# Kernel tuning notes

Hardware: AMD Instinct MI355X
Metric: run time of the kernel (lower is better)

Reference implementation:

```python
import jax, jax.numpy as jnp
import numpy as np

T, B, N = 12, 2, 1024
M = B * N            # nodes per timestep (batch-flattened)
D_IN, D_H, D_T, D_O = 64, 128, 16, 32


def _linear_params(k, fin, fout):
    kw, kb = jax.random.split(k)
    s = 1.0 / np.sqrt(fin)
    w = jax.random.uniform(kw, (fin, fout), jnp.float32, -s, s)
    b = jax.random.uniform(kb, (fout,), jnp.float32, -s, s)
    return w, b


def setup_inputs() -> dict:
    key = jax.random.key(0)
    ks = jax.random.split(key, 12)
    x = jax.random.normal(ks[0], (T, M, D_IN), jnp.float32)
    A = (jax.random.uniform(ks[1], (T, M, M)) < 0.01).astype(jnp.float32)
    A = A * (1.0 - jnp.eye(M, dtype=jnp.float32))  # no self-loops in raw adjacency
    ego_mask = jax.random.randint(ks[2], (B, T, N), 0, 2).astype(bool)
    gcn1_w, gcn1_b = _linear_params(ks[3], D_IN, D_H)
    gcn2_w, gcn2_b = _linear_params(ks[4], D_H, D_H)
    time_w, time_b = _linear_params(ks[5], 1, D_T)
    q_w, q_b = _linear_params(ks[6], D_H + D_T, D_H)
    k_w, k_b = _linear_params(ks[7], D_H + D_T, D_H)
    v_w, v_b = _linear_params(ks[8], D_H + D_T, D_H)
    o_w, o_b = _linear_params(ks[9], D_H, D_H)
    fc_w, fc_b = _linear_params(ks[10], D_H, D_O)
    return dict(x=x, A=A, ego_mask=ego_mask,
                gcn1_w=gcn1_w, gcn1_b=gcn1_b, gcn2_w=gcn2_w, gcn2_b=gcn2_b,
                time_w=time_w, time_b=time_b,
                q_w=q_w, q_b=q_b, k_w=k_w, k_b=k_b, v_w=v_w, v_b=v_b,
                o_w=o_w, o_b=o_b, fc_w=fc_w, fc_b=fc_b)


def _forward(x, A, ego_mask, gcn1_w, gcn1_b, gcn2_w, gcn2_b, time_w, time_b,
             q_w, q_b, k_w, k_b, v_w, v_b, o_w, o_b, fc_w, fc_b):
    # [B,T,N] -> [T, B*N], as in mask.permute(1,0,2).reshape(T,-1)
    mask = ego_mask.transpose(1, 0, 2).reshape(T, M)
    tvals = jnp.arange(T, dtype=jnp.float32)

    def step(_, inp):
        xt, At, mt, tv = inp  # [M,D_IN], [M,M], [M] bool, scalar
        m = mt.astype(xt.dtype)
        # restrict adjacency to masked subgraph; GCNConv adds self-loops
        A_hat = At * (m[:, None] * m[None, :]) + jnp.diag(m)
        deg = A_hat.sum(axis=0)  # in-degree per target (PyG gcn_norm on col)
        nrm = jnp.where(deg > 0, 1.0 / jnp.sqrt(jnp.maximum(deg, 1e-12)), 0.0)

        def gcn(h, w, b):
            # out[i] = nrm[i] * sum_j A_hat[j,i] * nrm[j] * (hW)[j] + b
            return (A_hat.T @ ((h @ w) * nrm[:, None])) * nrm[:, None] + b

        h = jax.nn.relu(gcn(xt, gcn1_w, gcn1_b))
        h = jax.nn.relu(gcn(h, gcn2_w, gcn2_b))
        # t_vec = sin(Linear(1,D_T)(t)) -- identical for all nodes
        t_vec = jnp.sin(tv * time_w[0] + time_b)  # [D_T]
        xtc = jnp.concatenate([h, jnp.broadcast_to(t_vec, (M, D_T))], axis=-1)
        Q = xtc @ q_w + q_b
        K = xtc @ k_w + k_b
        V = xtc @ v_w + v_b
        scores = (Q @ K.T) * (1.0 / np.sqrt(D_H))  # [M,M]
        scores = jnp.where(mt[None, :], scores, -1e9)  # keys restricted to mask
        agg = jax.nn.softmax(scores, axis=-1) @ V
        out = ((agg @ o_w + o_b) @ fc_w + fc_b) * m[:, None]  # scatter-back == mask
        return None, out

    _, outs = jax.lax.scan(step, None, (x, A, mask, tvals))  # [T,M,D_O]
    return outs.reshape(T, B, N, D_O).transpose(1, 2, 0, 3)  # [B,N,T,D_O]


def reference(x, A, ego_mask, gcn1_w, gcn1_b, gcn2_w, gcn2_b, time_w, time_b,
              q_w, q_b, k_w, k_b, v_w, v_b, o_w, o_b, fc_w, fc_b):
    return _forward(x, A, ego_mask, gcn1_w, gcn1_b, gcn2_w, gcn2_b, time_w,
                    time_b, q_w, q_b, k_w, k_b, v_w, v_b, o_w, o_b, fc_w, fc_b)
```

## Files before the change

kernel.cpp:

```cpp
#include <hip/hip_runtime.h>
#include <stdint.h>

#define TT   12
#define BB   2
#define NN   1024
#define MM   2048
#define TM   24576
#define DIN  64
#define DH   128
#define DOUT 32
#define CAP  64
#define OUTSZ 786432
#define KS   4
#define PWB  324

typedef __attribute__((ext_vector_type(8))) short short8;
typedef __attribute__((ext_vector_type(4))) short short4v;
typedef __attribute__((ext_vector_type(4))) float f32x4;

#define MFMA(a,b,c) __builtin_amdgcn_mfma_f32_16x16x32_bf16((a),(b),(c),0,0,0)

__device__ __forceinline__ float bf2f(unsigned short u){
  union { uint32_t i; float f; } x; x.i = ((uint32_t)u) << 16; return x.f;
}
__device__ __forceinline__ unsigned short f2bf(float f){
  union { float f; uint32_t i; } x; x.f = f;
  uint32_t u = x.i + 0x7FFFu + ((x.i >> 16) & 1u);
  return (unsigned short)(u >> 16);
}
__device__ __forceinline__ float LD(const void* p, size_t i, int mode){
  return mode ? ((const float*)p)[i] : bf2f(((const unsigned short*)p)[i]);
}
__device__ __forceinline__ short8 ldx8(const void* x, size_t off, int md){
  if(md){
    const float4* xf = (const float4*)((const float*)x + off);
    float4 a = xf[0], b = xf[1];
    short8 o;
    o[0]=(short)f2bf(a.x); o[1]=(short)f2bf(a.y); o[2]=(short)f2bf(a.z); o[3]=(short)f2bf(a.w);
    o[4]=(short)f2bf(b.x); o[5]=(short)f2bf(b.y); o[6]=(short)f2bf(b.z); o[7]=(short)f2bf(b.w);
    return o;
  }
  return *(const short8*)((const unsigned short*)x + off);
}

__global__ void k_fill(float* __restrict__ out, int n, float val){
  int i = blockIdx.x*blockDim.x + threadIdx.x;
  if(i < n) out[i] = val;
}

__global__ void k_detect2(const unsigned short* __restrict__ x,
                          const unsigned char* __restrict__ eg,
                          int* __restrict__ dtf, int* __restrict__ flag,
                          int* __restrict__ nact){
  if(blockIdx.x == 0){
    __shared__ int cnt_s;
    if(threadIdx.x==0) cnt_s = 0;
    if(threadIdx.x < TT) nact[threadIdx.x] = 0;
    __syncthreads();
    int c = 0;
    for(int i=threadIdx.x; i<6144; i+=blockDim.x){
      unsigned short h = x[i*2];
      unsigned e = (h >> 7) & 0xFF;
      if(h==0 || (e >= 0x60 && e <= 0x9F)) c++;
    }
    atomicAdd(&cnt_s, c);
    __syncthreads();
    if(threadIdx.x==0) *dtf = (cnt_s > 4000) ? 0 : 1;
  } else {
    __shared__ int pres_s, ge2_s;
    if(threadIdx.x==0){ pres_s=0; ge2_s=0; }
    __syncthreads();
    int pres=0, ge2=0;
    for(int i=threadIdx.x; i<24576; i+=blockDim.x){
      unsigned v = eg[i];
      if(v){ pres |= 1 << (i & 7); if(v >= 2u) ge2 = 1; }
    }
    if(pres) atomicOr(&pres_s, pres);
    if(ge2)  atomicOr(&ge2_s, 1);
    __syncthreads();
    if(threadIdx.x==0){
      int pr = pres_s, g2 = ge2_s, mode;
      if(!g2){
        if((pr & ~0x01) == 0)      mode = 4;
        else if((pr & ~0x11) == 0) mode = 0;
        else                       mode = 1;
      } else {
        if((pr & ~0xC0) == 0)      mode = 5;
        else if((pr & ~0xCC) == 0) mode = 3;
        else                       mode = 2;
      }
      *flag = mode;
    }
  }
}

__global__ void k_mask(const void* __restrict__ egom, const int* __restrict__ flag,
                       int* __restrict__ cnt, int* __restrict__ nact,
                       int* __restrict__ aidx, int* __restrict__ inv,
                       float* __restrict__ out){
  int idx = blockIdx.x*blockDim.x + threadIdx.x;
  out[idx] = 0.f;
  if(idx >= TM) return;
  int t = idx / MM, node = idx % MM;
  int b = node / NN, n = node % NN;
  int src = (b*TT + t)*NN + n;
  int mode = *flag;
  int v;
  if(mode==0)      v = ((const int*)egom)[src] != 0;
  else if(mode==1) v = ((const unsigned char*)egom)[src] != 0;
  else if(mode==2) v = ((const unsigned short*)egom)[src] != 0;
  else if(mode==3) v = ((const float*)egom)[src] != 0.f;
  else if(mode==4) v = ((const long long*)egom)[src] != 0;
  else             v = ((const double*)egom)[src] != 0.0;
  cnt[idx] = 0;
  unsigned long long bal = __ballot(v != 0);
  int lane = threadIdx.x & 63;
  int base = 0;
  if(lane == 0 && bal) base = atomicAdd(&nact[t], __popcll(bal));
  base = __shfl(base, 0, 64);
  int ic = -1;
  if(v){
    int pfx = __popcll(bal & ((1ULL << lane) - 1ULL));
    ic = base + pfx;
    aidx[(size_t)t*MM + ic] = node;
  }
  inv[idx] = ic;
}

__global__ __launch_bounds__(256) void k_prep_edges(
  const void* __restrict__ w1, const void* __restrict__ w2,
  const void* __restrict__ qw, const void* __restrict__ kw, const void* __restrict__ vw,
  const void* __restrict__ qb0, const void* __restrict__ kb0, const void* __restrict__ vb0,
  const void* __restrict__ ow, const void* __restrict__ ob,
  const void* __restrict__ fw, const void* __restrict__ fb,
  const void* __restrict__ tw, const void* __restrict__ tb,
  const void* __restrict__ b1, const void* __restrict__ b2,
  const int* __restrict__ dtf,
  unsigned short* __restrict__ W1t, unsigned short* __restrict__ W2t,
  unsigned short* __restrict__ Wqt, unsigned short* __restrict__ Wkt,
  unsigned short* __restrict__ Wvt, unsigned short* __restrict__ Wct,
  float* __restrict__ qbf, float* __restrict__ kbf, float* __restrict__ vbf,
  float* __restrict__ bcf, float* __restrict__ b1f, float* __restrict__ b2f,
  const void* __restrict__ A, const int* __restrict__ inv,
  int* __restrict__ cnt, int* __restrict__ edges)
{
  const int md = *dtf;
  if(blockIdx.x < PWB){
    int id = blockIdx.x*blockDim.x + threadIdx.x;
    if(id < 8192){
      int n=id&127, k2=id>>7; W1t[n*64+k2]=f2bf(LD(w1,(size_t)k2*128+n,md)); return; }
    id -= 8192;
    if(id < 16384){ int n=id&127,k2=id>>7; W2t[n*128+k2]=f2bf(LD(w2,(size_t)k2*128+n,md)); return; }
    id -= 16384;
    if(id < 16384){ int n=id&127,k2=id>>7; Wqt[n*128+k2]=f2bf(LD(qw,(size_t)k2*128+n,md)); return; }
    id -= 16384;
    if(id < 16384){ int n=id&127,k2=id>>7; Wkt[n*128+k2]=f2bf(LD(kw,(size_t)k2*128+n,md)); return; }
    id -= 16384;
    if(id < 16384){ int n=id&127,k2=id>>7; Wvt[n*128+k2]=f2bf(LD(vw,(size_t)k2*128+n,md)); return; }
    id -= 16384;
    if(id < 4096){
      int oc=id&31, c=id>>5; float s=0.f;
      for(int r=0;r<128;r++) s += LD(ow,(size_t)c*128+r,md)*LD(fw,(size_t)r*32+oc,md);
      Wct[oc*128+c]=f2bf(s); return;
    }
    id -= 4096;
    if(id < 32){
      float s = LD(fb,id,md);
      for(int r=0;r<128;r++) s += LD(ob,r,md)*LD(fw,(size_t)r*32+id,md);
      bcf[id]=s; return;
    }
    id -= 32;
    if(id < 4608){
      int which = id/1536, rem=id%1536, t=rem/128, n=rem%128;
      const void* W  = which==0?qw:(which==1?kw:vw);
      const void* Bs = which==0?qb0:(which==1?kb0:vb0);
      float s = LD(Bs,n,md);
      for(int d=0;d<16;d++){
        float tv = sinf((float)t*LD(tw,d,md) + LD(tb,d,md));
        s += tv * LD(W,(size_t)(128+d)*128+n,md);
      }
      float* dst = which==0?qbf:(which==1?kbf:vbf);
      dst[t*128+n]=s; return;
    }
    id -= 4608;
    if(id < 256){
      if(id<128) b1f[id] = LD(b1,id,md);
      else       b2f[id-128] = LD(b2,id-128,md);
      return;
    }
  } else {
    int id = (blockIdx.x - PWB)*blockDim.x + threadIdx.x;
    int seg = id & 63; int row = id >> 6;
    int t = row / MM;
    int jc = inv[row];
    if(jc < 0) return;
    const int* invt = inv + (size_t)t*MM;
    int* cb = cnt + (size_t)t*MM;
    int* eb = edges + (size_t)t*MM*CAP;
    if(md){
      const float4* p4 = (const float4*)((const float*)A + (size_t)row*MM + seg*32);
      #pragma unroll
      for(int u=0;u<8;u++){
        float4 v = p4[u];
        float wd[4]={v.x,v.y,v.z,v.w};
        #pragma unroll
        for(int q=0;q<4;q++){
          if(wd[q]!=0.f){
            int ibc = invt[seg*32 + u*4 + q];
            if(ibc >= 0){ int s=atomicAdd(&cb[ibc],1); if(s<CAP) eb[(size_t)ibc*CAP+s]=jc; }
          }
        }
      }
    } else {
      const uint4* p4 = (const uint4*)((const unsigned short*)A + (size_t)row*MM + seg*32);
      #pragma unroll
      for(int u=0;u<4;u++){
        uint4 v = p4[u];
        unsigned wd[4]={v.x,v.y,v.z,v.w};
        #pragma unroll
        for(int q=0;q<4;q++){
          int ib = seg*32 + u*8 + q*2;
          if(wd[q] & 0xFFFFu){
            int ibc = invt[ib];
            if(ibc >= 0){ int s=atomicAdd(&cb[ibc],1); if(s<CAP) eb[(size_t)ibc*CAP+s]=jc; }
          }
          if(wd[q] >> 16){
            int ibc = invt[ib+1];
            if(ibc >= 0){ int s=atomicAdd(&cb[ibc],1); if(s<CAP) eb[(size_t)ibc*CAP+s]=jc; }
          }
        }
      }
    }
  }
}

__global__ __launch_bounds__(256) void k_gemm_x(const void* __restrict__ x,
    const int* __restrict__ dtf, const int* __restrict__ nact,
    const int* __restrict__ aidx, const unsigned short* __restrict__ Wt,
    float* __restrict__ g)
{
  const int tile = blockIdx.x*64;
  const int t = tile / MM, il = tile % MM;
  const int na = nact[t];
  if(il >= ((na+63)&~63)) return;
  const int md = *dtf;
  const int tid=threadIdx.x, wv=tid>>6, lane=tid&63, l15=lane&15, quad=lane>>4;
  const int r0 = tile + (wv>>1)*32;
  const int c0 = (wv&1)*64;
  short8 bf[2][4];
  #pragma unroll
  for(int kk=0;kk<2;kk++)
    #pragma unroll
    for(int nt=0;nt<4;nt++)
      bf[kk][nt] = *(const short8*)(Wt + (size_t)(c0+nt*16+l15)*DIN + kk*32 + quad*8);
  const int il0 = (r0 % MM) + l15, il1 = (r0 % MM) + 16 + l15;
  const int n0 = aidx[(size_t)t*MM + (il0 < na ? il0 : 0)];
  const int n1 = aidx[(size_t)t*MM + (il1 < na ? il1 : 0)];
  const size_t xb0 = ((size_t)t*MM + n0)*DIN;
  const size_t xb1 = ((size_t)t*MM + n1)*DIN;
  f32x4 z = {0.f,0.f,0.f,0.f};
  f32x4 acc[2][4];
  #pragma unroll
  for(int i=0;i<2;i++){ acc[i][0]=z; acc[i][1]=z; acc[i][2]=z; acc[i][3]=z; }
  #pragma unroll
  for(int kk=0;kk<2;kk++){
    short8 a0 = ldx8(x, xb0 + kk*32 + quad*8, md);
    short8 a1 = ldx8(x, xb1 + kk*32 + quad*8, md);
    #pragma unroll
    for(int nt=0;nt<4;nt++){
      acc[0][nt]=MFMA(a0,bf[kk][nt],acc[0][nt]);
      acc[1][nt]=MFMA(a1,bf[kk][nt],acc[1][nt]);
    }
  }
  #pragma unroll
  for(int mt=0;mt<2;mt++)
    #pragma unroll
    for(int nt=0;nt<4;nt++){
      int col = c0+nt*16+l15;
      #pragma unroll
      for(int r=0;r<4;r++){
        int row = r0 + mt*16 + quad*4 + r;
        g[(size_t)row*DH + col] = acc[mt][nt][r];
      }
    }
}

__global__ __launch_bounds__(256) void k_gemm_h(const unsigned short* __restrict__ X,
    const unsigned short* __restrict__ Wt, float* __restrict__ g,
    const int* __restrict__ nact)
{
  const int tile = blockIdx.x*64;
  const int t = tile / MM, il = tile % MM;
  const int na = nact[t];
  if(il >= ((na+63)&~63)) return;
  const int tid=threadIdx.x, wv=tid>>6, lane=tid&63, l15=lane&15, quad=lane>>4;
  const int r0 = tile + (wv>>1)*32;
  const int c0 = (wv&1)*64;
  short8 bf[4][4];
  #pragma unroll
  for(int kk=0;kk<4;kk++)
    #pragma unroll
    for(int nt=0;nt<4;nt++)
      bf[kk][nt] = *(const short8*)(Wt + (size_t)(c0+nt*16+l15)*DH + kk*32 + quad*8);
  f32x4 z = {0.f,0.f,0.f,0.f};
  f32x4 acc[2][4];
  #pragma unroll
  for(int i=0;i<2;i++){ acc[i][0]=z; acc[i][1]=z; acc[i][2]=z; acc[i][3]=z; }
  #pragma unroll
  for(int kk=0;kk<4;kk++){
    short8 a0 = *(const short8*)(X + (size_t)(r0+l15)*DH    + kk*32 + quad*8);
    short8 a1 = *(const short8*)(X + (size_t)(r0+16+l15)*DH + kk*32 + quad*8);
    #pragma unroll
    for(int nt=0;nt<4;nt++){
      acc[0][nt]=MFMA(a0,bf[kk][nt],acc[0][nt]);
      acc[1][nt]=MFMA(a1,bf[kk][nt],acc[1][nt]);
    }
  }
  #pragma unroll
  for(int mt=0;mt<2;mt++)
    #pragma unroll
    for(int nt=0;nt<4;nt++){
      int col = c0+nt*16+l15;
      #pragma unroll
      for(int r=0;r<4;r++){
        int row = r0 + mt*16 + quad*4 + r;
        g[(size_t)row*DH + col] = acc[mt][nt][r];
      }
    }
}

__global__ __launch_bounds__(256) void k_gather(const float* __restrict__ g,
    const int* __restrict__ edges, const int* __restrict__ cnt,
    const int* __restrict__ nact, const float* __restrict__ bias,
    unsigned short* __restrict__ h)
{
  int wv = threadIdx.x>>6, lane = threadIdx.x&63;
  int gi = blockIdx.x*4 + wv;
  int t = gi / MM, ic = gi % MM;
  int na = nact[t];
  if(ic >= ((na+63)&~63)) return;
  unsigned int* hp = (unsigned int*)(h + (size_t)gi*DH) + lane;
  if(ic >= na){ *hp = 0; return; }
  float a0=0.f, a1=0.f;
  int cn = cnt[gi]; if(cn>CAP) cn=CAP;
  const int* eb = edges + (size_t)gi*CAP;
  #pragma unroll 2
  for(int e=0;e<cn;e++){
    int jc = eb[e];
    float nj = rsqrtf((float)cnt[(size_t)t*MM+jc] + 1.f);
    float2 gr2 = *(const float2*)(g + ((size_t)t*MM + jc)*DH + 2*lane);
    a0 += nj*gr2.x; a1 += nj*gr2.y;
  }
  float ni = rsqrtf((float)cn + 1.f);
  float2 gs2 = *(const float2*)(g + (size_t)gi*DH + 2*lane);
  float h0 = ni*(a0 + ni*gs2.x) + bias[2*lane];
  float h1 = ni*(a1 + ni*gs2.y) + bias[2*lane+1];
  h0 = h0>0.f?h0:0.f; h1 = h1>0.f?h1:0.f;
  *hp = (unsigned int)f2bf(h0) | ((unsigned int)f2bf(h1) << 16);
}

__global__ __launch_bounds__(256) void k_gemm_qkv(const unsigned short* __restrict__ X,
    const unsigned short* __restrict__ Wq, const unsigned short* __restrict__ Wk,
    const unsigned short* __restrict__ Wv,
    const float* __restrict__ qb, const float* __restrict__ kb, const float* __restrict__ vb,
    unsigned short* __restrict__ Qo, unsigned short* __restrict__ Ko,
    unsigned short* __restrict__ Vtc, const int* __restrict__ nact)
{
  const int tile = blockIdx.x*64;
  const int t = tile / MM, il = tile % MM;
  const int na = nact[t];
  if(il >= ((na+63)&~63)) return;
  const int which = blockIdx.z;
  const unsigned short* Wt = which==0?Wq:(which==1?Wk:Wv);
  const float* bias = which==0?qb:(which==1?kb:vb);
  const int tid=threadIdx.x, wv=tid>>6, lane=tid&63, l15=lane&15, quad=lane>>4;
  const int r0 = tile + (wv>>1)*32;
  const int c0 = (wv&1)*64;
  short8 bf[4][4];
  #pragma unroll
  for(int kk=0;kk<4;kk++)
    #pragma unroll
    for(int nt=0;nt<4;nt++)
      bf[kk][nt] = *(const short8*)(Wt + (size_t)(c0+nt*16+l15)*DH + kk*32 + quad*8);
  f32x4 z = {0.f,0.f,0.f,0.f};
  f32x4 acc[2][4];
  #pragma unroll
  for(int i=0;i<2;i++){ acc[i][0]=z; acc[i][1]=z; acc[i][2]=z; acc[i][3]=z; }
  #pragma unroll
  for(int kk=0;kk<4;kk++){
    short8 a0 = *(const short8*)(X + (size_t)(r0+l15)*DH    + kk*32 + quad*8);
    short8 a1 = *(const short8*)(X + (size_t)(r0+16+l15)*DH + kk*32 + quad*8);
    #pragma unroll
    for(int nt=0;nt<4;nt++){
      acc[0][nt]=MFMA(a0,bf[kk][nt],acc[0][nt]);
      acc[1][nt]=MFMA(a1,bf[kk][nt],acc[1][nt]);
    }
  }
  if(which < 2){
    unsigned short* o = which==0 ? Qo : Ko;
    #pragma unroll
    for(int mt=0;mt<2;mt++)
      #pragma unroll
      for(int nt=0;nt<4;nt++){
        int col = c0+nt*16+l15;
        float bb = bias[t*DH+col];
        #pragma unroll
        for(int r=0;r<4;r++){
          int row = r0 + mt*16 + quad*4 + r;
          o[(size_t)row*DH + col] = f2bf(acc[mt][nt][r] + bb);
        }
      }
  } else {
    #pragma unroll
    for(int mt=0;mt<2;mt++)
      #pragma unroll
      for(int nt=0;nt<4;nt++){
        int col = c0+nt*16+l15;
        float bb = bias[t*DH+col];
        int node0 = il + (wv>>1)*32 + mt*16 + quad*4;
        short4v pk;
        #pragma unroll
        for(int r=0;r<4;r++) pk[r] = (short)f2bf(acc[mt][nt][r] + bb);
        *(short4v*)(Vtc + ((size_t)t*DH + col)*MM + node0) = pk;
      }
  }
}

__global__ __launch_bounds__(256) void k_attn_part(
  const unsigned short* __restrict__ Q, const unsigned short* __restrict__ Kc,
  const unsigned short* __restrict__ Vtc, const int* __restrict__ nact,
  float* __restrict__ pacc, float* __restrict__ plr)
{
  __shared__ unsigned short Kl[64][136];
  __shared__ unsigned short Vl[128][72];
  __shared__ short Pl[4][16][72];
  const int tid=threadIdx.x, wv=tid>>6, lane=tid&63, l15=lane&15, quad=lane>>4;
  const int t = blockIdx.y, s = blockIdx.z;
  const int na = nact[t];
  const int qblk = blockIdx.x*64;
  if(qblk >= na) return;
  const int qbase = qblk + wv*16;
  const float scale = 0.088388347648318447f;
  const int nkt = (na + 63) >> 6;

  short8 bq[4];
  #pragma unroll
  for(int kk=0;kk<4;kk++)
    bq[kk] = *(const short8*)(Q + ((size_t)t*MM + qbase + l15)*DH + kk*32 + quad*8);

  f32x4 zz = {0.f,0.f,0.f,0.f};
  f32x4 accPV[8];
  #pragma unroll
  for(int i=0;i<8;i++) accPV[i]=zz;
  float l_run = 0.f;

  const int srow = tid >> 2, sseg = tid & 3;
  const int vch  = tid >> 1, vhalf = tid & 1;

  short8 kreg[4], vreg[4];
  if(s < nkt){
    const unsigned short* gk = Kc + ((size_t)t*MM + s*64 + srow)*DH + sseg*32;
    const unsigned short* gv = Vtc + ((size_t)t*DH + vch)*MM + s*64 + vhalf*32;
    #pragma unroll
    for(int j=0;j<4;j++){ kreg[j] = *(const short8*)(gk + j*8);
                          vreg[j] = *(const short8*)(gv + j*8); }
  }

  for(int kt=s; kt<nkt; kt+=KS){
    const int key0 = kt*64;
    __syncthreads();
    {
      short8* kd = (short8*)&Kl[srow][sseg*32];
      short8* vd = (short8*)&Vl[vch][vhalf*32];
      #pragma unroll
      for(int j=0;j<4;j++){ kd[j] = kreg[j]; vd[j] = vreg[j]; }
    }
    __syncthreads();
    if(kt+KS < nkt){
      const int key1 = key0 + KS*64;
      const unsigned short* gk = Kc + ((size_t)t*MM + key1 + srow)*DH + sseg*32;
      const unsigned short* gv = Vtc + ((size_t)t*DH + vch)*MM + key1 + vhalf*32;
      #pragma unroll
      for(int j=0;j<4;j++){ kreg[j] = *(const short8*)(gk + j*8);
                            vreg[j] = *(const short8*)(gv + j*8); }
    }
    #pragma unroll
    for(int mt=0;mt<4;mt++){
      f32x4 sv4 = zz;
      #pragma unroll
      for(int kk=0;kk<4;kk++){
        short8 ak = *(const short8*)&Kl[mt*16+l15][kk*32 + quad*8];
        sv4 = MFMA(ak, bq[kk], sv4);
      }
      short4v pk;
      #pragma unroll
      for(int r=0;r<4;r++){
        float sv = fminf(fmaxf(sv4[r]*scale, -15.f), 15.f);
        float valid = (key0 + mt*16 + quad*4 + r < na) ? 1.f : 0.f;
        float p = __expf(sv) * valid;
        pk[r] = (short)f2bf(p);
        l_run += bf2f((unsigned short)pk[r]);
      }
      *(short4v*)&Pl[wv][l15][mt*16 + quad*4] = pk;
    }
    #pragma unroll
    for(int kk=0;kk<2;kk++){
      short8 ap = *(const short8*)&Pl[wv][l15][kk*32 + quad*8];
      #pragma unroll
      for(int nt=0;nt<8;nt++){
        short8 bv = *(const short8*)&Vl[nt*16+l15][kk*32 + quad*8];
        accPV[nt] = MFMA(ap, bv, accPV[nt]);
      }
    }
  }
  float* pb = pacc + ((((size_t)s*TT + t)*32 + blockIdx.x)*256 + tid)*32;
  #pragma unroll
  for(int i=0;i<8;i++) *(f32x4*)(pb + i*4) = accPV[i];
  plr[(((size_t)s*TT + t)*32 + blockIdx.x)*256 + tid] = l_run;
}

__global__ __launch_bounds__(256) void k_attn_fin(
  const float* __restrict__ pacc, const float* __restrict__ plr,
  const int* __restrict__ nact, const int* __restrict__ aidx,
  const unsigned short* __restrict__ Wct, const float* __restrict__ bc,
  float* __restrict__ out)
{
  __shared__ short Al[4][16][136];
  const int tid=threadIdx.x, wv=tid>>6, lane=tid&63, l15=lane&15, quad=lane>>4;
  const int t = blockIdx.y;
  const int na = nact[t];
  const int qblk = blockIdx.x*64;
  if(qblk >= na) return;
  const int qbase = qblk + wv*16;

  f32x4 zz = {0.f,0.f,0.f,0.f};
  f32x4 acc[8];
  #pragma unroll
  for(int i=0;i<8;i++) acc[i]=zz;
  float l_run = 0.f;
  #pragma unroll
  for(int s=0;s<KS;s++){
    const f32x4* p = (const f32x4*)(pacc + ((((size_t)s*TT + t)*32 + blockIdx.x)*256 + tid)*32);
    #pragma unroll
    for(int i=0;i<8;i++) acc[i] += p[i];
    l_run += plr[(((size_t)s*TT + t)*32 + blockIdx.x)*256 + tid];
  }
  l_run += __shfl_xor(l_run, 16, 64);
  l_run += __shfl_xor(l_run, 32, 64);

  #pragma unroll
  for(int nt=0;nt<8;nt++)
    #pragma unroll
    for(int r=0;r<4;r++){
      float av = fminf(fmaxf(acc[nt][r], -1e30f), 1e30f);
      Al[wv][quad*4+r][nt*16+l15] = (short)f2bf(av);
    }

  const int qc = qbase + l15;
  const bool qok = (qc < na);
  const float linv = (l_run > 0.f) ? 1.f/l_run : 0.f;
  const int node = aidx[(size_t)t*MM + (qok ? qc : 0)];
  #pragma unroll
  for(int mt2=0;mt2<2;mt2++){
    f32x4 d = zz;
    #pragma unroll
    for(int kk=0;kk<4;kk++){
      short8 aw = *(const short8*)(Wct + (size_t)(mt2*16+l15)*DH + kk*32 + quad*8);
      short8 bl = *(const short8*)&Al[wv][l15][kk*32 + quad*8];
      d = MFMA(aw, bl, d);
    }
    f32x4 bcv = *(const f32x4*)(bc + mt2*16 + quad*4);
    f32x4 o4;
    #pragma unroll
    for(int r=0;r<4;r++) o4[r] = d[r]*linv + bcv[r];
    if(qok)
      *(f32x4*)(out + (size_t)node*(TT*DOUT) + (size_t)t*DOUT + mt2*16 + quad*4) = o4;
  }
}

extern "C" void kernel_launch(void* const* d_in, const int* in_sizes, int n_in,
                              void* d_out, int out_size, void* d_ws, size_t ws_size,
                              hipStream_t stream)
{
  float* outp = (float*)d_out;
  static const int EXP[19] = {1572864,50331648,24576,8192,128,16384,128,16,16,
                              18432,128,18432,128,18432,128,16384,128,4096,32};
  bool ok = (n_in >= 19) && (out_size == OUTSZ);
  if(ok) for(int i=0;i<19;i++) if(in_sizes[i] != EXP[i]) { ok = false; break; }
  if(!ok){
    k_fill<<<(out_size+255)/256,256,0,stream>>>(outp, out_size, 1000.f);
    return;
  }
  const void* x   = d_in[0];
  const void* A   = d_in[1];
  const void* eg  = d_in[2];
  const void* w1  = d_in[3];
  const void* b1  = d_in[4];
  const void* w2  = d_in[5];
  const void* b2  = d_in[6];
  const void* tw  = d_in[7];
  const void* tb  = d_in[8];
  const void* qw  = d_in[9];
  const void* qb0 = d_in[10];
  const void* kw  = d_in[11];
  const void* kb0 = d_in[12];
  const void* vw  = d_in[13];
  const void* vb0 = d_in[14];
  const void* ow  = d_in[15];
  const void* ob  = d_in[16];
  const void* fw  = d_in[17];
  const void* fb  = d_in[18];

  char* w = (char*)d_ws;
  size_t off = 0;
  auto alloc = [&](size_t sz)->char*{
    char* p = w + off; off = (off + sz + 255) & ~(size_t)255; return p; };
  int*   flag  = (int*)  alloc(4);
  int*   dtf   = (int*)  alloc(4);
  int*   nactb = (int*)  alloc(TT*4);
  int*   cnt   = (int*)  alloc((size_t)TM*4);
  int*   aidx  = (int*)  alloc((size_t)TM*4);
  int*   inv   = (int*)  alloc((size_t)TM*4);
  int*   edges = (int*)  alloc((size_t)TM*CAP*4);
  float* g     = (float*)alloc((size_t)TM*DH*4);
  unsigned short* h   = (unsigned short*)alloc((size_t)TM*DH*2);
  unsigned short* Vtc = (unsigned short*)alloc((size_t)TT*DH*MM*2);
  unsigned short* W1t = (unsigned short*)alloc(DH*DIN*2);
  unsigned short* W2t = (unsigned short*)alloc(DH*DH*2);
  unsigned short* Wqt = (unsigned short*)alloc(DH*DH*2);
  unsigned short* Wkt = (unsigned short*)alloc(DH*DH*2);
  unsigned short* Wvt = (unsigned short*)alloc(DH*DH*2);
  unsigned short* Wct = (unsigned short*)alloc(DOUT*DH*2);
  float* qbf = (float*)alloc(TT*DH*4);
  float* kbf = (float*)alloc(TT*DH*4);
  float* vbf = (float*)alloc(TT*DH*4);
  float* bcf = (float*)alloc(DOUT*4);
  float* b1f = (float*)alloc(DH*4);
  float* b2f = (float*)alloc(DH*4);
  float* pacc = (float*)alloc((size_t)KS*TT*32*256*32*4);
  float* plr  = (float*)alloc((size_t)KS*TT*32*256*4);
  if(off > ws_size){
    k_fill<<<(out_size+255)/256,256,0,stream>>>(outp, out_size, 500.f);
    return;
  }

  unsigned short* Qb = (unsigned short*)g;
  unsigned short* Kb = (unsigned short*)((char*)g + (size_t)TM*DH*2);

  k_detect2<<<2,256,0,stream>>>((const unsigned short*)x, (const unsigned char*)eg,
                                dtf, flag, nactb);
  k_mask<<<OUTSZ/256,256,0,stream>>>(eg, flag, cnt, nactb, aidx, inv, outp);
  k_prep_edges<<<PWB + TM*64/256,256,0,stream>>>(w1,w2,qw,kw,vw,qb0,kb0,vb0,ow,ob,fw,fb,tw,tb,
                                                 b1,b2,dtf,
                                                 W1t,W2t,Wqt,Wkt,Wvt,Wct,qbf,kbf,vbf,bcf,b1f,b2f,
                                                 A, inv, cnt, edges);
  k_gemm_x<<<TM/64,256,0,stream>>>(x, dtf, nactb, aidx, W1t, g);
  k_gather<<<TM/4,256,0,stream>>>(g, edges, cnt, nactb, b1f, h);
  k_gemm_h<<<TM/64,256,0,stream>>>(h, W2t, g, nactb);
  k_gather<<<TM/4,256,0,stream>>>(g, edges, cnt, nactb, b2f, h);
  k_gemm_qkv<<<dim3(TM/64,1,3),256,0,stream>>>(h, Wqt,Wkt,Wvt, qbf,kbf,vbf, Qb,Kb,Vtc, nactb);
  k_attn_part<<<dim3(MM/64,TT,KS),256,0,stream>>>(Qb, Kb, Vtc, nactb, pacc, plr);
  k_attn_fin<<<dim3(MM/64,TT),256,0,stream>>>(pacc, plr, nactb, aidx, Wct, bcf, outp);
}
```

Measured before the change: 507.9 us.

## Fuse all pipeline stages into one cooperative persistent kernel with grid syncs

Replaces the chain of about ten kernel launches with a single cooperative kernel of 768 persistent blocks. Each stage (detection, mask compaction, weight prep, edge build, GEMMs, gathers, QKV, attention partial and finalize) runs as a grid-strided task loop, with grid.sync between stages. The aim is to remove launch gaps and tail effects between the many small kernels. The cost is that every stage is limited to 768 resident blocks, the 45 KB shared-memory footprint and the launch bound may cap occupancy, and each grid barrier adds its own overhead. The old multi-kernel path is kept as a fallback if the cooperative launch fails.

```diff
diff --git a/kernel.cpp b/kernel.cpp
--- a/kernel.cpp
+++ b/kernel.cpp
@@ -1,5 +1,8 @@
 #include <hip/hip_runtime.h>
+#include <hip/hip_cooperative_groups.h>
 #include <stdint.h>
+
+namespace cg = cooperative_groups;
 
 #define TT   12
 #define BB   2
@@ -13,6 +16,7 @@
 #define OUTSZ 786432
 #define KS   4
 #define PWB  324
+#define GRID 768
 
 typedef __attribute__((ext_vector_type(8))) short short8;
 typedef __attribute__((ext_vector_type(4))) short short4v;
@@ -42,6 +46,468 @@
   }
   return *(const short8*)((const unsigned short*)x + off);
 }
+
+
+__device__ __forceinline__ void dev_mask_item(int idx, int mode, int lane,
+    const void* egom, int* cnt, int* nact, int* aidx, int* inv){
+  int t = idx / MM, node = idx % MM;
+  int b = node / NN, n = node % NN;
+  int src = (b*TT + t)*NN + n;
+  int v;
+  if(mode==0)      v = ((const int*)egom)[src] != 0;
+  else if(mode==1) v = ((const unsigned char*)egom)[src] != 0;
+  else if(mode==2) v = ((const unsigned short*)egom)[src] != 0;
+  else if(mode==3) v = ((const float*)egom)[src] != 0.f;
+  else if(mode==4) v = ((const long long*)egom)[src] != 0;
+  else             v = ((const double*)egom)[src] != 0.0;
+  cnt[idx] = 0;
+  unsigned long long bal = __ballot(v != 0);
+  int base = 0;
+  if(lane == 0 && bal) base = atomicAdd(&nact[t], __popcll(bal));
+  base = __shfl(base, 0, 64);
+  int ic = -1;
+  if(v){
+    int pfx = __popcll(bal & ((1ULL << lane) - 1ULL));
+    ic = base + pfx;
+    aidx[(size_t)t*MM + ic] = node;
+  }
+  inv[idx] = ic;
+}
+
+__device__ __forceinline__ void dev_prepw_item(int id, int md,
+  const void* w1, const void* w2,
+  const void* qw, const void* kw, const void* vw,
+  const void* qb0, const void* kb0, const void* vb0,
+  const void* ow, const void* ob, const void* fw, const void* fb,
+  const void* tw, const void* tb, const void* b1, const void* b2,
+  unsigned short* W1t, unsigned short* W2t,
+  unsigned short* Wqt, unsigned short* Wkt,
+  unsigned short* Wvt, unsigned short* Wct,
+  float* qbf, float* kbf, float* vbf,
+  float* bcf, float* b1f, float* b2f)
+{
+  if(id < 8192){
+    int n=id&127, k2=id>>7; W1t[n*64+k2]=f2bf(LD(w1,(size_t)k2*128+n,md)); return; }
+  id -= 8192;
+  if(id < 16384){ int n=id&127,k2=id>>7; W2t[n*128+k2]=f2bf(LD(w2,(size_t)k2*128+n,md)); return; }
+  id -= 16384;
+  if(id < 16384){ int n=id&127,k2=id>>7; Wqt[n*128+k2]=f2bf(LD(qw,(size_t)k2*128+n,md)); return; }
+  id -= 16384;
+  if(id < 16384){ int n=id&127,k2=id>>7; Wkt[n*128+k2]=f2bf(LD(kw,(size_t)k2*128+n,md)); return; }
+  id -= 16384;
+  if(id < 16384){ int n=id&127,k2=id>>7; Wvt[n*128+k2]=f2bf(LD(vw,(size_t)k2*128+n,md)); return; }
+  id -= 16384;
+  if(id < 4096){
+    int oc=id&31, c=id>>5; float s=0.f;
+    for(int r=0;r<128;r++) s += LD(ow,(size_t)c*128+r,md)*LD(fw,(size_t)r*32+oc,md);
+    Wct[oc*128+c]=f2bf(s); return;
+  }
+  id -= 4096;
+  if(id < 32){
+    float s = LD(fb,id,md);
+    for(int r=0;r<128;r++) s += LD(ob,r,md)*LD(fw,(size_t)r*32+id,md);
+    bcf[id]=s; return;
+  }
+  id -= 32;
+  if(id < 4608){
+    int which = id/1536, rem=id%1536, t=rem/128, n=rem%128;
+    const void* W  = which==0?qw:(which==1?kw:vw);
+    const void* Bs = which==0?qb0:(which==1?kb0:vb0);
+    float s = LD(Bs,n,md);
+    for(int d=0;d<16;d++){
+      float tv = sinf((float)t*LD(tw,d,md) + LD(tb,d,md));
+      s += tv * LD(W,(size_t)(128+d)*128+n,md);
+    }
+    float* dst = which==0?qbf:(which==1?kbf:vbf);
+    dst[t*128+n]=s; return;
+  }
+  id -= 4608;
+  if(id < 256){
+    if(id<128) b1f[id] = LD(b1,id,md);
+    else       b2f[id-128] = LD(b2,id-128,md);
+    return;
+  }
+}
+
+__device__ __forceinline__ void dev_edges_item(int id, int md,
+    const void* A, const int* inv, int* cnt, int* edges){
+  int seg = id & 63; int row = id >> 6;
+  int t = row / MM;
+  int jc = inv[row];
+  if(jc < 0) return;
+  const int* invt = inv + (size_t)t*MM;
+  int* cb = cnt + (size_t)t*MM;
+  int* eb = edges + (size_t)t*MM*CAP;
+  if(md){
+    const float4* p4 = (const float4*)((const float*)A + (size_t)row*MM + seg*32);
+    #pragma unroll
+    for(int u=0;u<8;u++){
+      float4 v = p4[u];
+      float wd[4]={v.x,v.y,v.z,v.w};
+      #pragma unroll
+      for(int q=0;q<4;q++){
+        if(wd[q]!=0.f){
+          int ibc = invt[seg*32 + u*4 + q];
+          if(ibc >= 0){ int s=atomicAdd(&cb[ibc],1); if(s<CAP) eb[(size_t)ibc*CAP+s]=jc; }
+        }
+      }
+    }
+  } else {
+    const uint4* p4 = (const uint4*)((const unsigned short*)A + (size_t)row*MM + seg*32);
+    #pragma unroll
+    for(int u=0;u<4;u++){
+      uint4 v = p4[u];
+      unsigned wd[4]={v.x,v.y,v.z,v.w};
+      #pragma unroll
+      for(int q=0;q<4;q++){
+        int ib = seg*32 + u*8 + q*2;
+        if(wd[q] & 0xFFFFu){
+          int ibc = invt[ib];
+          if(ibc >= 0){ int s=atomicAdd(&cb[ibc],1); if(s<CAP) eb[(size_t)ibc*CAP+s]=jc; }
+        }
+        if(wd[q] >> 16){
+          int ibc = invt[ib+1];
+          if(ibc >= 0){ int s=atomicAdd(&cb[ibc],1); if(s<CAP) eb[(size_t)ibc*CAP+s]=jc; }
+        }
+      }
+    }
+  }
+}
+
+__device__ __forceinline__ void dev_gemm_x_tile(int tileIdx, int md, int tid,
+    const void* x, const int* nact, const int* aidx,
+    const unsigned short* Wt, float* g)
+{
+  const int tile = tileIdx*64;
+  const int t = tile / MM, il = tile % MM;
+  const int na = nact[t];
+  if(il >= ((na+63)&~63)) return;
+  const int wv=tid>>6, lane=tid&63, l15=lane&15, quad=lane>>4;
+  const int r0 = tile + (wv>>1)*32;
+  const int c0 = (wv&1)*64;
+  short8 bf[2][4];
+  #pragma unroll
+  for(int kk=0;kk<2;kk++)
+    #pragma unroll
+    for(int nt=0;nt<4;nt++)
+      bf[kk][nt] = *(const short8*)(Wt + (size_t)(c0+nt*16+l15)*DIN + kk*32 + quad*8);
+  const int il0 = (r0 % MM) + l15, il1 = (r0 % MM) + 16 + l15;
+  const int n0 = aidx[(size_t)t*MM + (il0 < na ? il0 : 0)];
+  const int n1 = aidx[(size_t)t*MM + (il1 < na ? il1 : 0)];
+  const size_t xb0 = ((size_t)t*MM + n0)*DIN;
+  const size_t xb1 = ((size_t)t*MM + n1)*DIN;
+  f32x4 z = {0.f,0.f,0.f,0.f};
+  f32x4 acc[2][4];
+  #pragma unroll
+  for(int i=0;i<2;i++){ acc[i][0]=z; acc[i][1]=z; acc[i][2]=z; acc[i][3]=z; }
+  #pragma unroll
+  for(int kk=0;kk<2;kk++){
+    short8 a0 = ldx8(x, xb0 + kk*32 + quad*8, md);
+    short8 a1 = ldx8(x, xb1 + kk*32 + quad*8, md);
+    #pragma unroll
+    for(int nt=0;nt<4;nt++){
+      acc[0][nt]=MFMA(a0,bf[kk][nt],acc[0][nt]);
+      acc[1][nt]=MFMA(a1,bf[kk][nt],acc[1][nt]);
+    }
+  }
+  #pragma unroll
+  for(int mt=0;mt<2;mt++)
+    #pragma unroll
+    for(int nt=0;nt<4;nt++){
+      int col = c0+nt*16+l15;
+      #pragma unroll
+      for(int r=0;r<4;r++){
+        int row = r0 + mt*16 + quad*4 + r;
+        g[(size_t)row*DH + col] = acc[mt][nt][r];
+      }
+    }
+}
+
+__device__ __forceinline__ void dev_gemm_h_tile(int tileIdx, int tid,
+    const unsigned short* X, const unsigned short* Wt, float* g, const int* nact)
+{
+  const int tile = tileIdx*64;
+  const int t = tile / MM, il = tile % MM;
+  const int na = nact[t];
+  if(il >= ((na+63)&~63)) return;
+  const int wv=tid>>6, lane=tid&63, l15=lane&15, quad=lane>>4;
+  const int r0 = tile + (wv>>1)*32;
+  const int c0 = (wv&1)*64;
+  short8 bf[4][4];
+  #pragma unroll
+  for(int kk=0;kk<4;kk++)
+    #pragma unroll
+    for(int nt=0;nt<4;nt++)
+      bf[kk][nt] = *(const short8*)(Wt + (size_t)(c0+nt*16+l15)*DH + kk*32 + quad*8);
+  f32x4 z = {0.f,0.f,0.f,0.f};
+  f32x4 acc[2][4];
+  #pragma unroll
+  for(int i=0;i<2;i++){ acc[i][0]=z; acc[i][1]=z; acc[i][2]=z; acc[i][3]=z; }
+  #pragma unroll
+  for(int kk=0;kk<4;kk++){
+    short8 a0 = *(const short8*)(X + (size_t)(r0+l15)*DH    + kk*32 + quad*8);
+    short8 a1 = *(const short8*)(X + (size_t)(r0+16+l15)*DH + kk*32 + quad*8);
+    #pragma unroll
+    for(int nt=0;nt<4;nt++){
+      acc[0][nt]=MFMA(a0,bf[kk][nt],acc[0][nt]);
+      acc[1][nt]=MFMA(a1,bf[kk][nt],acc[1][nt]);
+    }
+  }
+  #pragma unroll
+  for(int mt=0;mt<2;mt++)
+    #pragma unroll
+    for(int nt=0;nt<4;nt++){
+      int col = c0+nt*16+l15;
+      #pragma unroll
+      for(int r=0;r<4;r++){
+        int row = r0 + mt*16 + quad*4 + r;
+        g[(size_t)row*DH + col] = acc[mt][nt][r];
+      }
+    }
+}
+
+__device__ __forceinline__ void dev_gather_task(int gi, int lane,
+    const float* g, const int* edges, const int* cnt,
+    const int* nact, const float* bias, unsigned short* h)
+{
+  int t = gi / MM, ic = gi % MM;
+  int na = nact[t];
+  if(ic >= ((na+63)&~63)) return;
+  unsigned int* hp = (unsigned int*)(h + (size_t)gi*DH) + lane;
+  if(ic >= na){ *hp = 0; return; }
+  float a0=0.f, a1=0.f;
+  int cn = cnt[gi]; if(cn>CAP) cn=CAP;
+  const int* eb = edges + (size_t)gi*CAP;
+  #pragma unroll 2
+  for(int e=0;e<cn;e++){
+    int jc = eb[e];
+    float nj = rsqrtf((float)cnt[(size_t)t*MM+jc] + 1.f);
+    float2 gr2 = *(const float2*)(g + ((size_t)t*MM + jc)*DH + 2*lane);
+    a0 += nj*gr2.x; a1 += nj*gr2.y;
+  }
+  float ni = rsqrtf((float)cn + 1.f);
+  float2 gs2 = *(const float2*)(g + (size_t)gi*DH + 2*lane);
+  float h0 = ni*(a0 + ni*gs2.x) + bias[2*lane];
+  float h1 = ni*(a1 + ni*gs2.y) + bias[2*lane+1];
+  h0 = h0>0.f?h0:0.f; h1 = h1>0.f?h1:0.f;
+  *hp = (unsigned int)f2bf(h0) | ((unsigned int)f2bf(h1) << 16);
+}
+
+__device__ __forceinline__ void dev_qkv_tile(int tileIdx, int which, int tid,
+    const unsigned short* X,
+    const unsigned short* Wq, const unsigned short* Wk, const unsigned short* Wv,
+    const float* qb, const float* kb, const float* vb,
+    unsigned short* Qo, unsigned short* Ko, unsigned short* Vtc, const int* nact)
+{
+  const int tile = tileIdx*64;
+  const int t = tile / MM, il = tile % MM;
+  const int na = nact[t];
+  if(il >= ((na+63)&~63)) return;
+  const unsigned short* Wt = which==0?Wq:(which==1?Wk:Wv);
+  const float* bias = which==0?qb:(which==1?kb:vb);
+  const int wv=tid>>6, lane=tid&63, l15=lane&15, quad=lane>>4;
+  const int r0 = tile + (wv>>1)*32;
+  const int c0 = (wv&1)*64;
+  short8 bf[4][4];
+  #pragma unroll
+  for(int kk=0;kk<4;kk++)
+    #pragma unroll
+    for(int nt=0;nt<4;nt++)
+      bf[kk][nt] = *(const short8*)(Wt + (size_t)(c0+nt*16+l15)*DH + kk*32 + quad*8);
+  f32x4 z = {0.f,0.f,0.f,0.f};
+  f32x4 acc[2][4];
+  #pragma unroll
+  for(int i=0;i<2;i++){ acc[i][0]=z; acc[i][1]=z; acc[i][2]=z; acc[i][3]=z; }
+  #pragma unroll
+  for(int kk=0;kk<4;kk++){
+    short8 a0 = *(const short8*)(X + (size_t)(r0+l15)*DH    + kk*32 + quad*8);
+    short8 a1 = *(const short8*)(X + (size_t)(r0+16+l15)*DH + kk*32 + quad*8);
+    #pragma unroll
+    for(int nt=0;nt<4;nt++){
+      acc[0][nt]=MFMA(a0,bf[kk][nt],acc[0][nt]);
+      acc[1][nt]=MFMA(a1,bf[kk][nt],acc[1][nt]);
+    }
+  }
+  if(which < 2){
+    unsigned short* o = which==0 ? Qo : Ko;
+    #pragma unroll
+    for(int mt=0;mt<2;mt++)
+      #pragma unroll
+      for(int nt=0;nt<4;nt++){
+        int col = c0+nt*16+l15;
+        float bb = bias[t*DH+col];
+        #pragma unroll
+        for(int r=0;r<4;r++){
+          int row = r0 + mt*16 + quad*4 + r;
+          o[(size_t)row*DH + col] = f2bf(acc[mt][nt][r] + bb);
+        }
+      }
+  } else {
+    #pragma unroll
+    for(int mt=0;mt<2;mt++)
+      #pragma unroll
+      for(int nt=0;nt<4;nt++){
+        int col = c0+nt*16+l15;
+        float bb = bias[t*DH+col];
+        int node0 = il + (wv>>1)*32 + mt*16 + quad*4;
+        short4v pk;
+        #pragma unroll
+        for(int r=0;r<4;r++) pk[r] = (short)f2bf(acc[mt][nt][r] + bb);
+        *(short4v*)(Vtc + ((size_t)t*DH + col)*MM + node0) = pk;
+      }
+  }
+}
+
+__device__ __forceinline__ void dev_attn_part_task(int qx, int t, int s, int tid,
+  unsigned char* smem,
+  const unsigned short* Q, const unsigned short* Kc, const unsigned short* Vtc,
+  const int* nact, float* pacc, float* plr)
+{
+  unsigned short (*Kl)[136] = (unsigned short(*)[136])smem;
+  unsigned short (*Vl)[72]  = (unsigned short(*)[72])(smem + 17408);
+  short (*Pl)[16][72]       = (short(*)[16][72])(smem + 35840);
+  const int wv=tid>>6, lane=tid&63, l15=lane&15, quad=lane>>4;
+  const int na = nact[t];
+  const int qblk = qx*64;
+  if(qblk >= na) return;
+  const int qbase = qblk + wv*16;
+  const float scale = 0.088388347648318447f;
+  const int nkt = (na + 63) >> 6;
+
+  short8 bq[4];
+  #pragma unroll
+  for(int kk=0;kk<4;kk++)
+    bq[kk] = *(const short8*)(Q + ((size_t)t*MM + qbase + l15)*DH + kk*32 + quad*8);
+
+  f32x4 zz = {0.f,0.f,0.f,0.f};
+  f32x4 accPV[8];
+  #pragma unroll
+  for(int i=0;i<8;i++) accPV[i]=zz;
+  float l_run = 0.f;
+
+  const int srow = tid >> 2, sseg = tid & 3;
+  const int vch  = tid >> 1, vhalf = tid & 1;
+
+  short8 kreg[4], vreg[4];
+  if(s < nkt){
+    const unsigned short* gk = Kc + ((size_t)t*MM + s*64 + srow)*DH + sseg*32;
+    const unsigned short* gv = Vtc + ((size_t)t*DH + vch)*MM + s*64 + vhalf*32;
+    #pragma unroll
+    for(int j=0;j<4;j++){ kreg[j] = *(const short8*)(gk + j*8);
+                          vreg[j] = *(const short8*)(gv + j*8); }
+  }
+
+  for(int kt=s; kt<nkt; kt+=KS){
+    const int key0 = kt*64;
+    __syncthreads();
+    {
+      short8* kd = (short8*)&Kl[srow][sseg*32];
+      short8* vd = (short8*)&Vl[vch][vhalf*32];
+      #pragma unroll
+      for(int j=0;j<4;j++){ kd[j] = kreg[j]; vd[j] = vreg[j]; }
+    }
+    __syncthreads();
+    if(kt+KS < nkt){
+      const int key1 = key0 + KS*64;
+      const unsigned short* gk = Kc + ((size_t)t*MM + key1 + srow)*DH + sseg*32;
+      const unsigned short* gv = Vtc + ((size_t)t*DH + vch)*MM + key1 + vhalf*32;
+      #pragma unroll
+      for(int j=0;j<4;j++){ kreg[j] = *(const short8*)(gk + j*8);
+                            vreg[j] = *(const short8*)(gv + j*8); }
+    }
+    #pragma unroll
+    for(int mt=0;mt<4;mt++){
+      f32x4 sv4 = zz;
+      #pragma unroll
+      for(int kk=0;kk<4;kk++){
+        short8 ak = *(const short8*)&Kl[mt*16+l15][kk*32 + quad*8];
+        sv4 = MFMA(ak, bq[kk], sv4);
+      }
+      short4v pk;
+      #pragma unroll
+      for(int r=0;r<4;r++){
+        float sv = fminf(fmaxf(sv4[r]*scale, -15.f), 15.f);
+        float valid = (key0 + mt*16 + quad*4 + r < na) ? 1.f : 0.f;
+        float p = __expf(sv) * valid;
+        pk[r] = (short)f2bf(p);
+        l_run += bf2f((unsigned short)pk[r]);
+      }
+      *(short4v*)&Pl[wv][l15][mt*16 + quad*4] = pk;
+    }
+    #pragma unroll
+    for(int kk=0;kk<2;kk++){
+      short8 ap = *(const short8*)&Pl[wv][l15][kk*32 + quad*8];
+      #pragma unroll
+      for(int nt=0;nt<8;nt++){
+        short8 bv = *(const short8*)&Vl[nt*16+l15][kk*32 + quad*8];
+        accPV[nt] = MFMA(ap, bv, accPV[nt]);
+      }
+    }
+  }
+  float* pb = pacc + ((((size_t)s*TT + t)*32 + qx)*256 + tid)*32;
+  #pragma unroll
+  for(int i=0;i<8;i++) *(f32x4*)(pb + i*4) = accPV[i];
+  plr[(((size_t)s*TT + t)*32 + qx)*256 + tid] = l_run;
+}
+
+__device__ __forceinline__ void dev_attn_fin_task(int qx, int t, int tid,
+  unsigned char* smem,
+  const float* pacc, const float* plr,
+  const int* nact, const int* aidx,
+  const unsigned short* Wct, const float* bc, float* out)
+{
+  short (*Al)[16][136] = (short(*)[16][136])smem;
+  const int wv=tid>>6, lane=tid&63, l15=lane&15, quad=lane>>4;
+  const int na = nact[t];
+  const int qblk = qx*64;
+  if(qblk >= na) return;
+  const int qbase = qblk + wv*16;
+
+  f32x4 zz = {0.f,0.f,0.f,0.f};
+  f32x4 acc[8];
+  #pragma unroll
+  for(int i=0;i<8;i++) acc[i]=zz;
+  float l_run = 0.f;
+  #pragma unroll
+  for(int s=0;s<KS;s++){
+    const f32x4* p = (const f32x4*)(pacc + ((((size_t)s*TT + t)*32 + qx)*256 + tid)*32);
+    #pragma unroll
+    for(int i=0;i<8;i++) acc[i] += p[i];
+    l_run += plr[(((size_t)s*TT + t)*32 + qx)*256 + tid];
+  }
+  l_run += __shfl_xor(l_run, 16, 64);
+  l_run += __shfl_xor(l_run, 32, 64);
+
+  #pragma unroll
+  for(int nt=0;nt<8;nt++)
+    #pragma unroll
+    for(int r=0;r<4;r++){
+      float av = fminf(fmaxf(acc[nt][r], -1e30f), 1e30f);
+      Al[wv][quad*4+r][nt*16+l15] = (short)f2bf(av);
+    }
+
+  const int qc = qbase + l15;
+  const bool qok = (qc < na);
+  const float linv = (l_run > 0.f) ? 1.f/l_run : 0.f;
+  const int node = aidx[(size_t)t*MM + (qok ? qc : 0)];
+  #pragma unroll
+  for(int mt2=0;mt2<2;mt2++){
+    f32x4 d = zz;
+    #pragma unroll
+    for(int kk=0;kk<4;kk++){
+      short8 aw = *(const short8*)(Wct + (size_t)(mt2*16+l15)*DH + kk*32 + quad*8);
+      short8 bl = *(const short8*)&Al[wv][l15][kk*32 + quad*8];
+      d = MFMA(aw, bl, d);
+    }
+    f32x4 bcv = *(const f32x4*)(bc + mt2*16 + quad*4);
+    f32x4 o4;
+    #pragma unroll
+    for(int r=0;r<4;r++) o4[r] = d[r]*linv + bcv[r];
+    if(qok)
+      *(f32x4*)(out + (size_t)node*(TT*DOUT) + (size_t)t*DOUT + mt2*16 + quad*4) = o4;
+  }
+}
+
 
 __global__ void k_fill(float* __restrict__ out, int n, float val){
   int i = blockIdx.x*blockDim.x + threadIdx.x;
@@ -101,30 +567,7 @@
   int idx = blockIdx.x*blockDim.x + threadIdx.x;
   out[idx] = 0.f;
   if(idx >= TM) return;
-  int t = idx / MM, node = idx % MM;
-  int b = node / NN, n = node % NN;
-  int src = (b*TT + t)*NN + n;
-  int mode = *flag;
-  int v;
-  if(mode==0)      v = ((const int*)egom)[src] != 0;
-  else if(mode==1) v = ((const unsigned char*)egom)[src] != 0;
-  else if(mode==2) v = ((const unsigned short*)egom)[src] != 0;
-  else if(mode==3) v = ((const float*)egom)[src] != 0.f;
-  else if(mode==4) v = ((const long long*)egom)[src] != 0;
-  else             v = ((const double*)egom)[src] != 0.0;
-  cnt[idx] = 0;
-  unsigned long long bal = __ballot(v != 0);
-  int lane = threadIdx.x & 63;
-  int base = 0;
-  if(lane == 0 && bal) base = atomicAdd(&nact[t], __popcll(bal));
-  base = __shfl(base, 0, 64);
-  int ic = -1;
-  if(v){
-    int pfx = __popcll(bal & ((1ULL << lane) - 1ULL));
-    ic = base + pfx;
-    aidx[(size_t)t*MM + ic] = node;
-  }
-  inv[idx] = ic;
+  dev_mask_item(idx, *flag, threadIdx.x & 63, egom, cnt, nact, aidx, inv);
 }
 
 __global__ __launch_bounds__(256) void k_prep_edges(
@@ -147,90 +590,11 @@
   const int md = *dtf;
   if(blockIdx.x < PWB){
     int id = blockIdx.x*blockDim.x + threadIdx.x;
-    if(id < 8192){
-      int n=id&127, k2=id>>7; W1t[n*64+k2]=f2bf(LD(w1,(size_t)k2*128+n,md)); return; }
-    id -= 8192;
-    if(id < 16384){ int n=id&127,k2=id>>7; W2t[n*128+k2]=f2bf(LD(w2,(size_t)k2*128+n,md)); return; }
-    id -= 16384;
-    if(id < 16384){ int n=id&127,k2=id>>7; Wqt[n*128+k2]=f2bf(LD(qw,(size_t)k2*128+n,md)); return; }
-    id -= 16384;
-    if(id < 16384){ int n=id&127,k2=id>>7; Wkt[n*128+k2]=f2bf(LD(kw,(size_t)k2*128+n,md)); return; }
-    id -= 16384;
-    if(id < 16384){ int n=id&127,k2=id>>7; Wvt[n*128+k2]=f2bf(LD(vw,(size_t)k2*128+n,md)); return; }
-    id -= 16384;
-    if(id < 4096){
-      int oc=id&31, c=id>>5; float s=0.f;
-      for(int r=0;r<128;r++) s += LD(ow,(size_t)c*128+r,md)*LD(fw,(size_t)r*32+oc,md);
-      Wct[oc*128+c]=f2bf(s); return;
-    }
-    id -= 4096;
-    if(id < 32){
-      float s = LD(fb,id,md);
-      for(int r=0;r<128;r++) s += LD(ob,r,md)*LD(fw,(size_t)r*32+id,md);
-      bcf[id]=s; return;
-    }
-    id -= 32;
-    if(id < 4608){
-      int which = id/1536, rem=id%1536, t=rem/128, n=rem%128;
-      const void* W  = which==0?qw:(which==1?kw:vw);
-      const void* Bs = which==0?qb0:(which==1?kb0:vb0);
-      float s = LD(Bs,n,md);
-      for(int d=0;d<16;d++){
-        float tv = sinf((float)t*LD(tw,d,md) + LD(tb,d,md));
-        s += tv * LD(W,(size_t)(128+d)*128+n,md);
-      }
-      float* dst = which==0?qbf:(which==1?kbf:vbf);
-      dst[t*128+n]=s; return;
-    }
-    id -= 4608;
-    if(id < 256){
-      if(id<128) b1f[id] = LD(b1,id,md);
-      else       b2f[id-128] = LD(b2,id-128,md);
-      return;
-    }
+    dev_prepw_item(id, md, w1,w2,qw,kw,vw,qb0,kb0,vb0,ow,ob,fw,fb,tw,tb,b1,b2,
+                   W1t,W2t,Wqt,Wkt,Wvt,Wct,qbf,kbf,vbf,bcf,b1f,b2f);
   } else {
     int id = (blockIdx.x - PWB)*blockDim.x + threadIdx.x;
-    int seg = id & 63; int row = id >> 6;
-    int t = row / MM;
-    int jc = inv[row];
-    if(jc < 0) return;
-    const int* invt = inv + (size_t)t*MM;
-    int* cb = cnt + (size_t)t*MM;
-    int* eb = edges + (size_t)t*MM*CAP;
-    if(md){
-      const float4* p4 = (const float4*)((const float*)A + (size_t)row*MM + seg*32);
-      #pragma unroll
-      for(int u=0;u<8;u++){
-        float4 v = p4[u];
-        float wd[4]={v.x,v.y,v.z,v.w};
-        #pragma unroll
-        for(int q=0;q<4;q++){
-          if(wd[q]!=0.f){
-            int ibc = invt[seg*32 + u*4 + q];
-            if(ibc >= 0){ int s=atomicAdd(&cb[ibc],1); if(s<CAP) eb[(size_t)ibc*CAP+s]=jc; }
-          }
-        }
-      }
-    } else {
-      const uint4* p4 = (const uint4*)((const unsigned short*)A + (size_t)row*MM + seg*32);
-      #pragma unroll
-      for(int u=0;u<4;u++){
-        uint4 v = p4[u];
-        unsigned wd[4]={v.x,v.y,v.z,v.w};
-        #pragma unroll
-        for(int q=0;q<4;q++){
-          int ib = seg*32 + u*8 + q*2;
-          if(wd[q] & 0xFFFFu){
-            int ibc = invt[ib];
-            if(ibc >= 0){ int s=atomicAdd(&cb[ibc],1); if(s<CAP) eb[(size_t)ibc*CAP+s]=jc; }
-          }
-          if(wd[q] >> 16){
-            int ibc = invt[ib+1];
-            if(ibc >= 0){ int s=atomicAdd(&cb[ibc],1); if(s<CAP) eb[(size_t)ibc*CAP+s]=jc; }
-          }
-        }
-      }
-    }
+    dev_edges_item(id, md, A, inv, cnt, edges);
   }
 }
 
@@ -239,94 +603,14 @@
     const int* __restrict__ aidx, const unsigned short* __restrict__ Wt,
     float* __restrict__ g)
 {
-  const int tile = blockIdx.x*64;
-  const int t = tile / MM, il = tile % MM;
-  const int na = nact[t];
-  if(il >= ((na+63)&~63)) return;
-  const int md = *dtf;
-  const int tid=threadIdx.x, wv=tid>>6, lane=tid&63, l15=lane&15, quad=lane>>4;
-  const int r0 = tile + (wv>>1)*32;
-  const int c0 = (wv&1)*64;
-  short8 bf[2][4];
-  #pragma unroll
-  for(int kk=0;kk<2;kk++)
-    #pragma unroll
-    for(int nt=0;nt<4;nt++)
-      bf[kk][nt] = *(const short8*)(Wt + (size_t)(c0+nt*16+l15)*DIN + kk*32 + quad*8);
-  const int il0 = (r0 % MM) + l15, il1 = (r0 % MM) + 16 + l15;
-  const int n0 = aidx[(size_t)t*MM + (il0 < na ? il0 : 0)];
-  const int n1 = aidx[(size_t)t*MM + (il1 < na ? il1 : 0)];
-  const size_t xb0 = ((size_t)t*MM + n0)*DIN;
-  const size_t xb1 = ((size_t)t*MM + n1)*DIN;
-  f32x4 z = {0.f,0.f,0.f,0.f};
-  f32x4 acc[2][4];
-  #pragma unroll
-  for(int i=0;i<2;i++){ acc[i][0]=z; acc[i][1]=z; acc[i][2]=z; acc[i][3]=z; }
-  #pragma unroll
-  for(int kk=0;kk<2;kk++){
-    short8 a0 = ldx8(x, xb0 + kk*32 + quad*8, md);
-    short8 a1 = ldx8(x, xb1 + kk*32 + quad*8, md);
-    #pragma unroll
-    for(int nt=0;nt<4;nt++){
-      acc[0][nt]=MFMA(a0,bf[kk][nt],acc[0][nt]);
-      acc[1][nt]=MFMA(a1,bf[kk][nt],acc[1][nt]);
-    }
-  }
-  #pragma unroll
-  for(int mt=0;mt<2;mt++)
-    #pragma unroll
-    for(int nt=0;nt<4;nt++){
-      int col = c0+nt*16+l15;
-      #pragma unroll
-      for(int r=0;r<4;r++){
-        int row = r0 + mt*16 + quad*4 + r;
-        g[(size_t)row*DH + col] = acc[mt][nt][r];
-      }
-    }
+  dev_gemm_x_tile(blockIdx.x, *dtf, threadIdx.x, x, nact, aidx, Wt, g);
 }
 
 __global__ __launch_bounds__(256) void k_gemm_h(const unsigned short* __restrict__ X,
     const unsigned short* __restrict__ Wt, float* __restrict__ g,
     const int* __restrict__ nact)
 {
-  const int tile = blockIdx.x*64;
-  const int t = tile / MM, il = tile % MM;
-  const int na = nact[t];
-  if(il >= ((na+63)&~63)) return;
-  const int tid=threadIdx.x, wv=tid>>6, lane=tid&63, l15=lane&15, quad=lane>>4;
-  const int r0 = tile + (wv>>1)*32;
-  const int c0 = (wv&1)*64;
-  short8 bf[4][4];
-  #pragma unroll
-  for(int kk=0;kk<4;kk++)
-    #pragma unroll
-    for(int nt=0;nt<4;nt++)
-      bf[kk][nt] = *(const short8*)(Wt + (size_t)(c0+nt*16+l15)*DH + kk*32 + quad*8);
-  f32x4 z = {0.f,0.f,0.f,0.f};
-  f32x4 acc[2][4];
-  #pragma unroll
-  for(int i=0;i<2;i++){ acc[i][0]=z; acc[i][1]=z; acc[i][2]=z; acc[i][3]=z; }
-  #pragma unroll
-  for(int kk=0;kk<4;kk++){
-    short8 a0 = *(const short8*)(X + (size_t)(r0+l15)*DH    + kk*32 + quad*8);
-    short8 a1 = *(const short8*)(X + (size_t)(r0+16+l15)*DH + kk*32 + quad*8);
-    #pragma unroll
-    for(int nt=0;nt<4;nt++){
-      acc[0][nt]=MFMA(a0,bf[kk][nt],acc[0][nt]);
-      acc[1][nt]=MFMA(a1,bf[kk][nt],acc[1][nt]);
-    }
-  }
-  #pragma unroll
-  for(int mt=0;mt<2;mt++)
-    #pragma unroll
-    for(int nt=0;nt<4;nt++){
-      int col = c0+nt*16+l15;
-      #pragma unroll
-      for(int r=0;r<4;r++){
-        int row = r0 + mt*16 + quad*4 + r;
-        g[(size_t)row*DH + col] = acc[mt][nt][r];
-      }
-    }
+  dev_gemm_h_tile(blockIdx.x, threadIdx.x, X, Wt, g, nact);
 }
 
 __global__ __launch_bounds__(256) void k_gather(const float* __restrict__ g,
@@ -335,28 +619,7 @@
     unsigned short* __restrict__ h)
 {
   int wv = threadIdx.x>>6, lane = threadIdx.x&63;
-  int gi = blockIdx.x*4 + wv;
-  int t = gi / MM, ic = gi % MM;
-  int na = nact[t];
-  if(ic >= ((na+63)&~63)) return;
-  unsigned int* hp = (unsigned int*)(h + (size_t)gi*DH) + lane;
-  if(ic >= na){ *hp = 0; return; }
-  float a0=0.f, a1=0.f;
-  int cn = cnt[gi]; if(cn>CAP) cn=CAP;
-  const int* eb = edges + (size_t)gi*CAP;
-  #pragma unroll 2
-  for(int e=0;e<cn;e++){
-    int jc = eb[e];
-    float nj = rsqrtf((float)cnt[(size_t)t*MM+jc] + 1.f);
-    float2 gr2 = *(const float2*)(g + ((size_t)t*MM + jc)*DH + 2*lane);
-    a0 += nj*gr2.x; a1 += nj*gr2.y;
-  }
-  float ni = rsqrtf((float)cn + 1.f);
-  float2 gs2 = *(const float2*)(g + (size_t)gi*DH + 2*lane);
-  float h0 = ni*(a0 + ni*gs2.x) + bias[2*lane];
-  float h1 = ni*(a1 + ni*gs2.y) + bias[2*lane+1];
-  h0 = h0>0.f?h0:0.f; h1 = h1>0.f?h1:0.f;
-  *hp = (unsigned int)f2bf(h0) | ((unsigned int)f2bf(h1) << 16);
+  dev_gather_task(blockIdx.x*4 + wv, lane, g, edges, cnt, nact, bias, h);
 }
 
 __global__ __launch_bounds__(256) void k_gemm_qkv(const unsigned short* __restrict__ X,
@@ -366,64 +629,7 @@
     unsigned short* __restrict__ Qo, unsigned short* __restrict__ Ko,
     unsigned short* __restrict__ Vtc, const int* __restrict__ nact)
 {
-  const int tile = blockIdx.x*64;
-  const int t = tile / MM, il = tile % MM;
-  const int na = nact[t];
-  if(il >= ((na+63)&~63)) return;
-  const int which = blockIdx.z;
-  const unsigned short* Wt = which==0?Wq:(which==1?Wk:Wv);
-  const float* bias = which==0?qb:(which==1?kb:vb);
-  const int tid=threadIdx.x, wv=tid>>6, lane=tid&63, l15=lane&15, quad=lane>>4;
-  const int r0 = tile + (wv>>1)*32;
-  const int c0 = (wv&1)*64;
-  short8 bf[4][4];
-  #pragma unroll
-  for(int kk=0;kk<4;kk++)
-    #pragma unroll
-    for(int nt=0;nt<4;nt++)
-      bf[kk][nt] = *(const short8*)(Wt + (size_t)(c0+nt*16+l15)*DH + kk*32 + quad*8);
-  f32x4 z = {0.f,0.f,0.f,0.f};
-  f32x4 acc[2][4];
-  #pragma unroll
-  for(int i=0;i<2;i++){ acc[i][0]=z; acc[i][1]=z; acc[i][2]=z; acc[i][3]=z; }
-  #pragma unroll
-  for(int kk=0;kk<4;kk++){
-    short8 a0 = *(const short8*)(X + (size_t)(r0+l15)*DH    + kk*32 + quad*8);
-    short8 a1 = *(const short8*)(X + (size_t)(r0+16+l15)*DH + kk*32 + quad*8);
-    #pragma unroll
-    for(int nt=0;nt<4;nt++){
-      acc[0][nt]=MFMA(a0,bf[kk][nt],acc[0][nt]);
-      acc[1][nt]=MFMA(a1,bf[kk][nt],acc[1][nt]);
-    }
-  }
-  if(which < 2){
-    unsigned short* o = which==0 ? Qo : Ko;
-    #pragma unroll
-    for(int mt=0;mt<2;mt++)
-      #pragma unroll
-      for(int nt=0;nt<4;nt++){
-        int col = c0+nt*16+l15;
-        float bb = bias[t*DH+col];
-        #pragma unroll
-        for(int r=0;r<4;r++){
-          int row = r0 + mt*16 + quad*4 + r;
-          o[(size_t)row*DH + col] = f2bf(acc[mt][nt][r] + bb);
-        }
-      }
-  } else {
-    #pragma unroll
-    for(int mt=0;mt<2;mt++)
-      #pragma unroll
-      for(int nt=0;nt<4;nt++){
-        int col = c0+nt*16+l15;
-        float bb = bias[t*DH+col];
-        int node0 = il + (wv>>1)*32 + mt*16 + quad*4;
-        short4v pk;
-        #pragma unroll
-        for(int r=0;r<4;r++) pk[r] = (short)f2bf(acc[mt][nt][r] + bb);
-        *(short4v*)(Vtc + ((size_t)t*DH + col)*MM + node0) = pk;
-      }
-  }
+  dev_qkv_tile(blockIdx.x, blockIdx.z, threadIdx.x, X, Wq,Wk,Wv, qb,kb,vb, Qo,Ko,Vtc, nact);
 }
 
 __global__ __launch_bounds__(256) void k_attn_part(
@@ -431,92 +637,9 @@
   const unsigned short* __restrict__ Vtc, const int* __restrict__ nact,
   float* __restrict__ pacc, float* __restrict__ plr)
 {
-  __shared__ unsigned short Kl[64][136];
-  __shared__ unsigned short Vl[128][72];
-  __shared__ short Pl[4][16][72];
-  const int tid=threadIdx.x, wv=tid>>6, lane=tid&63, l15=lane&15, quad=lane>>4;
-  const int t = blockIdx.y, s = blockIdx.z;
-  const int na = nact[t];
-  const int qblk = blockIdx.x*64;
-  if(qblk >= na) return;
-  const int qbase = qblk + wv*16;
-  const float scale = 0.088388347648318447f;
-  const int nkt = (na + 63) >> 6;
-
-  short8 bq[4];
-  #pragma unroll
-  for(int kk=0;kk<4;kk++)
-    bq[kk] = *(const short8*)(Q + ((size_t)t*MM + qbase + l15)*DH + kk*32 + quad*8);
-
-  f32x4 zz = {0.f,0.f,0.f,0.f};
-  f32x4 accPV[8];
-  #pragma unroll
-  for(int i=0;i<8;i++) accPV[i]=zz;
-  float l_run = 0.f;
-
-  const int srow = tid >> 2, sseg = tid & 3;
-  const int vch  = tid >> 1, vhalf = tid & 1;
-
-  short8 kreg[4], vreg[4];
-  if(s < nkt){
-    const unsigned short* gk = Kc + ((size_t)t*MM + s*64 + srow)*DH + sseg*32;
-    const unsigned short* gv = Vtc + ((size_t)t*DH + vch)*MM + s*64 + vhalf*32;
-    #pragma unroll
-    for(int j=0;j<4;j++){ kreg[j] = *(const short8*)(gk + j*8);
-                          vreg[j] = *(const short8*)(gv + j*8); }
-  }
-
-  for(int kt=s; kt<nkt; kt+=KS){
-    const int key0 = kt*64;
-    __syncthreads();
-    {
-      short8* kd = (short8*)&Kl[srow][sseg*32];
-      short8* vd = (short8*)&Vl[vch][vhalf*32];
-      #pragma unroll
-      for(int j=0;j<4;j++){ kd[j] = kreg[j]; vd[j] = vreg[j]; }
-    }
-    __syncthreads();
-    if(kt+KS < nkt){
-      const int key1 = key0 + KS*64;
-      const unsigned short* gk = Kc + ((size_t)t*MM + key1 + srow)*DH + sseg*32;
-      const unsigned short* gv = Vtc + ((size_t)t*DH + vch)*MM + key1 + vhalf*32;
-      #pragma unroll
-      for(int j=0;j<4;j++){ kreg[j] = *(const short8*)(gk + j*8);
-                            vreg[j] = *(const short8*)(gv + j*8); }
-    }
-    #pragma unroll
-    for(int mt=0;mt<4;mt++){
-      f32x4 sv4 = zz;
-      #pragma unroll
-      for(int kk=0;kk<4;kk++){
-        short8 ak = *(const short8*)&Kl[mt*16+l15][kk*32 + quad*8];
-        sv4 = MFMA(ak, bq[kk], sv4);
-      }
-      short4v pk;
-      #pragma unroll
-      for(int r=0;r<4;r++){
-        float sv = fminf(fmaxf(sv4[r]*scale, -15.f), 15.f);
-        float valid = (key0 + mt*16 + quad*4 + r < na) ? 1.f : 0.f;
-        float p = __expf(sv) * valid;
-        pk[r] = (short)f2bf(p);
-        l_run += bf2f((unsigned short)pk[r]);
-      }
-      *(short4v*)&Pl[wv][l15][mt*16 + quad*4] = pk;
-    }
-    #pragma unroll
-    for(int kk=0;kk<2;kk++){
-      short8 ap = *(const short8*)&Pl[wv][l15][kk*32 + quad*8];
-      #pragma unroll
-      for(int nt=0;nt<8;nt++){
-        short8 bv = *(const short8*)&Vl[nt*16+l15][kk*32 + quad*8];
-        accPV[nt] = MFMA(ap, bv, accPV[nt]);
-      }
-    }
-  }
-  float* pb = pacc + ((((size_t)s*TT + t)*32 + blockIdx.x)*256 + tid)*32;
-  #pragma unroll
-  for(int i=0;i<8;i++) *(f32x4*)(pb + i*4) = accPV[i];
-  plr[(((size_t)s*TT + t)*32 + blockIdx.x)*256 + tid] = l_run;
+  __shared__ alignas(16) unsigned char smem[45056];
+  dev_attn_part_task(blockIdx.x, blockIdx.y, blockIdx.z, threadIdx.x, smem,
+                     Q, Kc, Vtc, nact, pacc, plr);
 }
 
 __global__ __launch_bounds__(256) void k_attn_fin(
@@ -525,58 +648,132 @@
   const unsigned short* __restrict__ Wct, const float* __restrict__ bc,
   float* __restrict__ out)
 {
-  __shared__ short Al[4][16][136];
-  const int tid=threadIdx.x, wv=tid>>6, lane=tid&63, l15=lane&15, quad=lane>>4;
-  const int t = blockIdx.y;
-  const int na = nact[t];
-  const int qblk = blockIdx.x*64;
-  if(qblk >= na) return;
-  const int qbase = qblk + wv*16;
-
-  f32x4 zz = {0.f,0.f,0.f,0.f};
-  f32x4 acc[8];
-  #pragma unroll
-  for(int i=0;i<8;i++) acc[i]=zz;
-  float l_run = 0.f;
-  #pragma unroll
-  for(int s=0;s<KS;s++){
-    const f32x4* p = (const f32x4*)(pacc + ((((size_t)s*TT + t)*32 + blockIdx.x)*256 + tid)*32);
-    #pragma unroll
-    for(int i=0;i<8;i++) acc[i] += p[i];
-    l_run += plr[(((size_t)s*TT + t)*32 + blockIdx.x)*256 + tid];
-  }
-  l_run += __shfl_xor(l_run, 16, 64);
-  l_run += __shfl_xor(l_run, 32, 64);
-
-  #pragma unroll
-  for(int nt=0;nt<8;nt++)
-    #pragma unroll
-    for(int r=0;r<4;r++){
-      float av = fminf(fmaxf(acc[nt][r], -1e30f), 1e30f);
-      Al[wv][quad*4+r][nt*16+l15] = (short)f2bf(av);
-    }
-
-  const int qc = qbase + l15;
-  const bool qok = (qc < na);
-  const float linv = (l_run > 0.f) ? 1.f/l_run : 0.f;
-  const int node = aidx[(size_t)t*MM + (qok ? qc : 0)];
-  #pragma unroll
-  for(int mt2=0;mt2<2;mt2++){
-    f32x4 d = zz;
-    #pragma unroll
-    for(int kk=0;kk<4;kk++){
-      short8 aw = *(const short8*)(Wct + (size_t)(mt2*16+l15)*DH + kk*32 + quad*8);
-      short8 bl = *(const short8*)&Al[wv][l15][kk*32 + quad*8];
-      d = MFMA(aw, bl, d);
-    }
-    f32x4 bcv = *(const f32x4*)(bc + mt2*16 + quad*4);
-    f32x4 o4;
-    #pragma unroll
-    for(int r=0;r<4;r++) o4[r] = d[r]*linv + bcv[r];
-    if(qok)
-      *(f32x4*)(out + (size_t)node*(TT*DOUT) + (size_t)t*DOUT + mt2*16 + quad*4) = o4;
-  }
-}
+  __shared__ alignas(16) unsigned char smem[17408];
+  dev_attn_fin_task(blockIdx.x, blockIdx.y, threadIdx.x, smem,
+                    pacc, plr, nact, aidx, Wct, bc, out);
+}
+
+
+struct MegaArgs {
+  const void *x, *A, *eg;
+  const void *w1, *b1, *w2, *b2, *tw, *tb;
+  const void *qw, *qb0, *kw, *kb0, *vw, *vb0, *ow, *ob, *fw, *fb;
+  int *nact, *cnt, *aidx, *inv, *edges;
+  float* g; unsigned short* h; unsigned short* Vtc;
+  unsigned short *W1t,*W2t,*Wqt,*Wkt,*Wvt,*Wct;
+  float *qbf,*kbf,*vbf,*bcf,*b1f,*b2f;
+  float *pacc,*plr;
+  unsigned short *Qb,*Kb;
+  float* out;
+};
+
+__global__ __launch_bounds__(256, 3) void k_mega(MegaArgs a){
+  cg::grid_group grid = cg::this_grid();
+  __shared__ alignas(16) unsigned char smem[45056];
+  const int tid = threadIdx.x, bid = blockIdx.x, G = gridDim.x;
+  const int lane = tid & 63;
+
+  int md, mode;
+  {
+    int* sh = (int*)smem;
+    if(tid < 3) sh[tid] = 0;
+    __syncthreads();
+    int c = 0;
+    const unsigned short* xs = (const unsigned short*)a.x;
+    for(int i=tid; i<6144; i+=256){
+      unsigned short hh = xs[i*2];
+      unsigned e = (hh >> 7) & 0xFF;
+      if(hh==0 || (e >= 0x60 && e <= 0x9F)) c++;
+    }
+    if(c) atomicAdd(&sh[0], c);
+    int pres=0, ge2=0;
+    const unsigned char* egp = (const unsigned char*)a.eg;
+    for(int i=tid; i<24576; i+=256){
+      unsigned v = egp[i];
+      if(v){ pres |= 1 << (i & 7); if(v >= 2u) ge2 = 1; }
+    }
+    if(pres) atomicOr(&sh[1], pres);
+    if(ge2)  atomicOr(&sh[2], 1);
+    __syncthreads();
+    md = (sh[0] > 4000) ? 0 : 1;
+    int pr = sh[1], g2 = sh[2];
+    if(!g2){
+      if((pr & ~0x01) == 0)      mode = 4;
+      else if((pr & ~0x11) == 0) mode = 0;
+      else                       mode = 1;
+    } else {
+      if((pr & ~0xC0) == 0)      mode = 5;
+      else if((pr & ~0xCC) == 0) mode = 3;
+      else                       mode = 2;
+    }
+    if(bid == 0 && tid < TT) a.nact[tid] = 0;
+    __syncthreads();
+  }
+  grid.sync();
+
+  {
+    const int D0 = TM, D1 = TM + 82720, DTOT = D1 + OUTSZ/4;
+    for(int base = bid*256; base < DTOT; base += G*256){
+      int id = base + tid;
+      if(id < D0){
+        dev_mask_item(id, mode, lane, a.eg, a.cnt, a.nact, a.aidx, a.inv);
+      } else if(id < D1){
+        dev_prepw_item(id - D0, md, a.w1,a.w2,a.qw,a.kw,a.vw,a.qb0,a.kb0,a.vb0,
+                       a.ow,a.ob,a.fw,a.fb,a.tw,a.tb,a.b1,a.b2,
+                       a.W1t,a.W2t,a.Wqt,a.Wkt,a.Wvt,a.Wct,
+                       a.qbf,a.kbf,a.vbf,a.bcf,a.b1f,a.b2f);
+      } else if(id < DTOT){
+        float4 z4; z4.x=0.f; z4.y=0.f; z4.z=0.f; z4.w=0.f;
+        ((float4*)a.out)[id - D1] = z4;
+      }
+    }
+  }
+  grid.sync();
+
+  {
+    const int EB = TM*64/256;
+    for(int task = bid; task < EB + 384; task += G){
+      if(task < EB) dev_edges_item(task*256 + tid, md, a.A, a.inv, a.cnt, a.edges);
+      else          dev_gemm_x_tile(task - EB, md, tid, a.x, a.nact, a.aidx, a.W1t, a.g);
+    }
+  }
+  grid.sync();
+
+  {
+    const int wv = tid >> 6;
+    for(int task = bid; task < TM/4; task += G)
+      dev_gather_task(task*4 + wv, lane, a.g, a.edges, a.cnt, a.nact, a.b1f, a.h);
+  }
+  grid.sync();
+
+  for(int task = bid; task < TM/64; task += G)
+    dev_gemm_h_tile(task, tid, a.h, a.W2t, a.g, a.nact);
+  grid.sync();
+
+  {
+    const int wv = tid >> 6;
+    for(int task = bid; task < TM/4; task += G)
+      dev_gather_task(task*4 + wv, lane, a.g, a.edges, a.cnt, a.nact, a.b2f, a.h);
+  }
+  grid.sync();
+
+  for(int task = bid; task < 3*(TM/64); task += G)
+    dev_qkv_tile(task % (TM/64), task / (TM/64), tid, a.h,
+                 a.Wqt, a.Wkt, a.Wvt, a.qbf, a.kbf, a.vbf, a.Qb, a.Kb, a.Vtc, a.nact);
+  grid.sync();
+
+  for(int task = bid; task < 32*TT*KS; task += G){
+    int qx = task / (TT*KS), rem = task % (TT*KS);
+    dev_attn_part_task(qx, rem / KS, rem % KS, tid, smem,
+                       a.Qb, a.Kb, a.Vtc, a.nact, a.pacc, a.plr);
+  }
+  grid.sync();
+
+  for(int task = bid; task < 32*TT; task += G)
+    dev_attn_fin_task(task / TT, task % TT, tid, smem,
+                      a.pacc, a.plr, a.nact, a.aidx, a.Wct, a.bcf, a.out);
+}
+
 
 extern "C" void kernel_launch(void* const* d_in, const int* in_sizes, int n_in,
                               void* d_out, int out_size, void* d_ws, size_t ws_size,
@@ -647,6 +844,22 @@
   unsigned short* Qb = (unsigned short*)g;
   unsigned short* Kb = (unsigned short*)((char*)g + (size_t)TM*DH*2);
 
+  MegaArgs ma;
+  ma.x=x; ma.A=A; ma.eg=eg;
+  ma.w1=w1; ma.b1=b1; ma.w2=w2; ma.b2=b2; ma.tw=tw; ma.tb=tb;
+  ma.qw=qw; ma.qb0=qb0; ma.kw=kw; ma.kb0=kb0; ma.vw=vw; ma.vb0=vb0;
+  ma.ow=ow; ma.ob=ob; ma.fw=fw; ma.fb=fb;
+  ma.nact=nactb; ma.cnt=cnt; ma.aidx=aidx; ma.inv=inv; ma.edges=edges;
+  ma.g=g; ma.h=h; ma.Vtc=Vtc;
+  ma.W1t=W1t; ma.W2t=W2t; ma.Wqt=Wqt; ma.Wkt=Wkt; ma.Wvt=Wvt; ma.Wct=Wct;
+  ma.qbf=qbf; ma.kbf=kbf; ma.vbf=vbf; ma.bcf=bcf; ma.b1f=b1f; ma.b2f=b2f;
+  ma.pacc=pacc; ma.plr=plr; ma.Qb=Qb; ma.Kb=Kb; ma.out=outp;
+  void* kp[] = { (void*)&ma };
+  hipError_t err = hipLaunchCooperativeKernel((const void*)k_mega,
+                                              dim3(GRID), dim3(256), kp, 0, stream);
+  if(err == hipSuccess) return;
+  (void)hipGetLastError();
+
   k_detect2<<<2,256,0,stream>>>((const unsigned short*)x, (const unsigned char*)eg,
                                 dtf, flag, nactb);
   k_mask<<<OUTSZ/256,256,0,stream>>>(eg, flag, cnt, nactb, aidx, inv, outp);
```

After: 1.246 ms. 145% more time.
